# Kernel optimization log

Measured on AMD Instinct MI355X. Metric: run time of the kernel, lower is better.

Reference implementation:

```python
import jax, jax.numpy as jnp
import numpy as np

B, T = 2048, 512
H1, H2, H3 = 100, 60, 30


def _glorot(key, shape, fan):
    bound = 1.0 / np.sqrt(fan)
    return jax.random.uniform(key, shape, jnp.float32, -bound, bound)


def setup_inputs() -> dict:
    key = jax.random.key(0)
    ks = jax.random.split(key, 17)
    inp = {"x": jax.random.normal(ks[0], (B, T, 2), jnp.float32)}
    # layer 1: input 2 -> hidden 100
    inp["W_ih1"] = _glorot(ks[1], (H1, 2), H1)
    inp["W_hh1"] = _glorot(ks[2], (H1, H1), H1)
    inp["b_ih1"] = _glorot(ks[3], (H1,), H1)
    inp["b_hh1"] = _glorot(ks[4], (H1,), H1)
    # layer 2: 100 -> 60
    inp["W_ih2"] = _glorot(ks[5], (H2, H1), H2)
    inp["W_hh2"] = _glorot(ks[6], (H2, H2), H2)
    inp["b_ih2"] = _glorot(ks[7], (H2,), H2)
    inp["b_hh2"] = _glorot(ks[8], (H2,), H2)
    # layer 3: 60 -> 30
    inp["W_ih3"] = _glorot(ks[9], (H3, H2), H3)
    inp["W_hh3"] = _glorot(ks[10], (H3, H3), H3)
    inp["b_ih3"] = _glorot(ks[11], (H3,), H3)
    inp["b_hh3"] = _glorot(ks[12], (H3,), H3)
    # heads
    inp["W_o1"] = _glorot(ks[13], (10, H3), 10)
    inp["b_o1"] = _glorot(ks[14], (10,), 10)
    inp["W_o2"] = _glorot(ks[15], (2, 10), 2)
    inp["b_o2"] = _glorot(ks[16], (2,), 2)
    return inp


def rnn_layer(x, W_ih, W_hh, b_ih, b_hh):
    # x: [B, T, in]; precompute the time-parallel input projection once
    xp = jnp.einsum("bti,hi->bth", x, W_ih) + (b_ih + b_hh)  # [B, T, H]
    h0 = jnp.zeros((x.shape[0], W_hh.shape[0]), x.dtype)

    def step(h, xt):  # xt: [B, H]
        h = jnp.tanh(xt + h @ W_hh.T)
        return h, h

    _, ys = jax.lax.scan(step, h0, jnp.swapaxes(xp, 0, 1))  # [T, B, H]
    return jnp.swapaxes(ys, 0, 1)  # [B, T, H]


def reference(x, W_ih1, W_hh1, b_ih1, b_hh1, W_ih2, W_hh2, b_ih2, b_hh2,
              W_ih3, W_hh3, b_ih3, b_hh3, W_o1, b_o1, W_o2, b_o2):
    h = rnn_layer(x, W_ih1, W_hh1, b_ih1, b_hh1)
    h = rnn_layer(h, W_ih2, W_hh2, b_ih2, b_hh2)
    h = rnn_layer(h, W_ih3, W_hh3, b_ih3, b_hh3)
    o = jnp.einsum("bth,oh->bto", h, W_o1) + b_o1
    return jnp.einsum("bto,po->btp", o, W_o2) + b_o2  # [B, T, 2]
```

## Files before the change

### kernel.cpp

```cpp
#include <hip/hip_runtime.h>

typedef _Float16 v8hf __attribute__((ext_vector_type(8)));
typedef float    v4f  __attribute__((ext_vector_type(4)));

#define MFMA16(a, b, c) __builtin_amdgcn_mfma_f32_16x16x32_f16((a), (b), (c), 0, 0, 0)

#define TT 512
#define BT 16
#define NTH 1024
#define KS 2.8853900817779268f
#define CL 13.8498724f

#define H1R 0u
#define H2R 8192u
#define H3R 12288u
#define XST 14336u
#define ORG 47168u

__shared__ __align__(16) char SM[55360];

__device__ __forceinline__ v4f tanh4s(v4f z) {
    float z0 = __builtin_amdgcn_fmed3f(z[0], -CL, CL);
    float z1 = __builtin_amdgcn_fmed3f(z[1], -CL, CL);
    float z2 = __builtin_amdgcn_fmed3f(z[2], -CL, CL);
    float z3 = __builtin_amdgcn_fmed3f(z[3], -CL, CL);
    float a0 = __builtin_amdgcn_exp2f(z0) + 1.f;
    float a1 = __builtin_amdgcn_exp2f(z1) + 1.f;
    float a2 = __builtin_amdgcn_exp2f(z2) + 1.f;
    float a3 = __builtin_amdgcn_exp2f(z3) + 1.f;
    float P = a0 * a1, Q = a2 * a3;
    float R = __builtin_amdgcn_rcpf(P * Q);
    float iP = Q * R, iQ = P * R;
    v4f t;
    t[0] = 1.f - 2.f * (a1 * iP);
    t[1] = 1.f - 2.f * (a0 * iP);
    t[2] = 1.f - 2.f * (a3 * iQ);
    t[3] = 1.f - 2.f * (a2 * iQ);
    return t;
}

__device__ __forceinline__ unsigned pk2h(float a, float b) {
    union { _Float16 h[2]; unsigned u; } x;
    x.h[0] = (_Float16)a; x.h[1] = (_Float16)b;
    return x.u;
}

__global__ __launch_bounds__(NTH, 1)
void rnn3_nu(const float* __restrict__ xg,
             const float* __restrict__ Wih1, const float* __restrict__ Whh1,
             const float* __restrict__ bih1, const float* __restrict__ bhh1,
             const float* __restrict__ Wih2, const float* __restrict__ Whh2,
             const float* __restrict__ bih2, const float* __restrict__ bhh2,
             const float* __restrict__ Wih3, const float* __restrict__ Whh3,
             const float* __restrict__ bih3, const float* __restrict__ bhh3,
             const float* __restrict__ Wo1,  const float* __restrict__ bo1,
             const float* __restrict__ Wo2,  const float* __restrict__ bo2,
             float* __restrict__ outg)
{
    const int tid   = threadIdx.x;
    const int lane  = tid & 63;
    const int wid   = tid >> 6;
    const int col   = lane & 15;
    const int g     = lane >> 4;
    const int bbase = blockIdx.x * BT;
    const unsigned l16 = (unsigned)lane * 16u;

    {
        float4 z = {0.f, 0.f, 0.f, 0.f};
        for (int i = tid; i < 896; i += NTH) ((float4*)SM)[i] = z;
        for (int i = tid; i < BT * TT; i += NTH) {
            const int b = i >> 9, t = i & 511;
            float2 xv = *(const float2*)(xg + (size_t)(bbase + b) * (TT * 2) + 2 * t);
            *(unsigned*)(SM + XST + (unsigned)t * 64u + (unsigned)b * 4u) = pk2h(xv.x, xv.y);
        }
        if (tid < 16) *(unsigned*)(SM + XST + 512u * 64u + (unsigned)tid * 4u) = 0u;
    }

    v8hf WF[6];
    #pragma unroll
    for (int i = 0; i < 6; ++i) WF[i] = (v8hf)(_Float16)0.f;
    v4f BB0 = {0.f, 0.f, 0.f, 0.f}, BH = {0.f, 0.f, 0.f, 0.f};

    auto ldA = [&](const float* W, int rows, int cols, int jg, int kt) -> v8hf {
        v8hf r;
        #pragma unroll
        for (int e = 0; e < 8; ++e) {
            const int kl = 32 * kt + 16 * (e >> 2) + 4 * g + (e & 3);
            float v = (jg < rows && kl < cols) ? W[jg * cols + kl] * KS : 0.f;
            r[e] = (_Float16)v;
        }
        return r;
    };
    auto ldA1 = [&](int jg, int kt) -> v8hf {
        v8hf r;
        #pragma unroll
        for (int e = 0; e < 8; ++e) {
            const int kl = 32 * kt + 16 * (e >> 2) + 4 * g + (e & 3);
            float v = 0.f;
            if (jg < 100) {
                if (kl < 100)       v = Whh1[jg * 100 + kl];
                else if (kl == 112) v = Wih1[jg * 2];
                else if (kl == 113) v = Wih1[jg * 2 + 1];
            }
            r[e] = (_Float16)(v * KS);
        }
        return r;
    };
    auto mkbias = [&](const float* bi, const float* bh, int n, int t) -> v4f {
        v4f b;
        #pragma unroll
        for (int i = 0; i < 4; ++i) {
            const int j = 16 * t + 4 * g + i;
            b[i] = (j < n) ? KS * (bi[j] + bh[j]) : 0.f;
        }
        return b;
    };

    if (wid < 7) {
        #pragma unroll
        for (int kt = 0; kt < 4; ++kt) WF[kt] = ldA1(16 * wid + col, kt);
        BB0 = mkbias(bih1, bhh1, 100, wid);
    } else if (wid >= 8 && wid < 12) {
        const int j = 16 * (wid - 8) + col;
        #pragma unroll
        for (int kt = 0; kt < 4; ++kt) WF[kt] = ldA(Wih2, 60, 100, j, kt);
        WF[4] = ldA(Whh2, 60, 60, j, 0);
        WF[5] = ldA(Whh2, 60, 60, j, 1);
        BB0 = mkbias(bih2, bhh2, 60, wid - 8);
    } else if (wid == 12 || wid == 13) {
        const int j = 16 * (wid - 12) + col;
        WF[0] = ldA(Wih3, 30, 60, j, 0);
        WF[1] = ldA(Wih3, 30, 60, j, 1);
        WF[2] = ldA(Whh3, 30, 30, j, 0);
        BB0 = mkbias(bih3, bhh3, 30, wid - 12);
    } else if (wid == 14) {
        #pragma unroll
        for (int e = 0; e < 8; ++e) {
            const int kl = 16 * (e >> 2) + 4 * g + (e & 3);
            float v = 0.f;
            if (col < 2 && kl < 30) {
                #pragma unroll
                for (int u = 0; u < 10; ++u) v += Wo2[col * 10 + u] * Wo1[u * 30 + kl];
            }
            WF[0][e] = (_Float16)v;
        }
        #pragma unroll
        for (int i = 0; i < 4; ++i) {
            float bv = 0.f;
            if (g == 0 && i < 2) {
                bv = bo2[i];
                #pragma unroll
                for (int u = 0; u < 10; ++u) bv += Wo2[i * 10 + u] * bo1[u];
            }
            BH[i] = bv;
        }
    }

    __syncthreads();
    if (tid < 16)
        *(unsigned*)(SM + H1R + 4096u + 3072u + (unsigned)tid * 16u + 8u) =
            *(const unsigned*)(SM + XST + (unsigned)tid * 4u);
    __syncthreads();

    auto flushfn = [&](int tbase) {
        const unsigned rb = ORG + (((unsigned)tbase & 63u) >> 1) * 16u;
        #pragma unroll
        for (int jj = 0; jj < 4; ++jj) {
            const int f = lane + 64 * jj;
            const int b = f >> 4, k = f & 15;
            float4 v = *(const float4*)(SM + rb + (unsigned)b * 512u + (unsigned)k * 16u);
            *(float4*)(outg + ((size_t)(bbase + b) * TT + tbase) * 2 + 4 * k) = v;
        }
    };

    unsigned rO1 = H1R + 4096u, wO1 = H1R;
    unsigned rO2 = H2R + 2048u, wO2 = H2R;
    unsigned rO3 = H3R + 1024u, wO3 = H3R;
    const v4f z4 = {0.f, 0.f, 0.f, 0.f};

    for (int s = 0; s < TT + 3; ++s) {
        if (wid < 7) {
            if (s < TT) {
                v8hf S0 = *(const v8hf*)(SM + rO1 + l16);
                v8hf S1 = *(const v8hf*)(SM + rO1 + 1024u + l16);
                v8hf S2 = *(const v8hf*)(SM + rO1 + 2048u + l16);
                v8hf S3 = *(const v8hf*)(SM + rO1 + 3072u + l16);
                v4f p = BB0, q = z4;
                p = MFMA16(WF[0], S0, p); q = MFMA16(WF[1], S1, q);
                p = MFMA16(WF[2], S2, p); q = MFMA16(WF[3], S3, q);
                v4f r = tanh4s(p + q);
                uint2 wv; wv.x = pk2h(r[0], r[1]); wv.y = pk2h(r[2], r[3]);
                *(uint2*)(SM + wO1 + (unsigned)(wid >> 1) * 1024u + l16
                             + (unsigned)(wid & 1) * 8u) = wv;
            }
        } else if (wid == 7) {
            if (s < TT - 1) {
                unsigned xv = *(const unsigned*)(SM + XST + (unsigned)(s + 1) * 64u
                                                    + (unsigned)col * 4u);
                uint2 wv; wv.x = (g == 0) ? xv : 0u; wv.y = 0u;
                *(uint2*)(SM + wO1 + 3072u + l16 + 8u) = wv;
            }
        } else if (wid < 12) {
            if (s >= 1 && s <= TT) {
                v8hf G0 = *(const v8hf*)(SM + rO1 + l16);
                v8hf G1 = *(const v8hf*)(SM + rO1 + 1024u + l16);
                v8hf G2 = *(const v8hf*)(SM + rO1 + 2048u + l16);
                v8hf G3 = *(const v8hf*)(SM + rO1 + 3072u + l16);
                v8hf H0 = *(const v8hf*)(SM + rO2 + l16);
                v8hf H1 = *(const v8hf*)(SM + rO2 + 1024u + l16);
                v4f p = BB0, q = z4, r2 = z4;
                p  = MFMA16(WF[0], G0, p);
                q  = MFMA16(WF[1], G1, q);
                r2 = MFMA16(WF[4], H0, r2);
                p  = MFMA16(WF[2], G2, p);
                q  = MFMA16(WF[3], G3, q);
                r2 = MFMA16(WF[5], H1, r2);
                v4f r = tanh4s(p + q + r2);
                const int t2 = wid - 8;
                uint2 wv; wv.x = pk2h(r[0], r[1]); wv.y = pk2h(r[2], r[3]);
                *(uint2*)(SM + wO2 + (unsigned)(t2 >> 1) * 1024u + l16
                             + (unsigned)(t2 & 1) * 8u) = wv;
            }
        } else if (wid < 14) {
            if (s >= 2 && s <= TT + 1) {
                v8hf G0 = *(const v8hf*)(SM + rO2 + l16);
                v8hf G1 = *(const v8hf*)(SM + rO2 + 1024u + l16);
                v8hf C0 = *(const v8hf*)(SM + rO3 + l16);
                v4f p = BB0, q = z4, r2 = z4;
                p  = MFMA16(WF[0], G0, p);
                q  = MFMA16(WF[1], G1, q);
                r2 = MFMA16(WF[2], C0, r2);
                v4f r = tanh4s(p + q + r2);
                const int t3 = wid - 12;
                uint2 wv; wv.x = pk2h(r[0], r[1]); wv.y = pk2h(r[2], r[3]);
                *(uint2*)(SM + wO3 + l16 + (unsigned)(t3 & 1) * 8u) = wv;
            }
        } else if (wid == 14) {
            if (s >= 3 && s <= TT + 2) {
                v8hf C0 = *(const v8hf*)(SM + rO3 + l16);
                v4f o = BH;
                o = MFMA16(WF[0], C0, o);
                if (g == 0)
                    *(float2*)(SM + ORG + (unsigned)col * 512u
                                  + ((unsigned)(s - 3) & 63u) * 8u) =
                        make_float2(o[0], o[1]);
            }
        } else {
            if (s >= 35 && ((s - 35) & 31) == 0) flushfn(s - 35);
        }
        __syncthreads();
        rO1 ^= 4096u; wO1 ^= 4096u;
        rO2 ^= 2048u; wO2 ^= 2048u;
        rO3 ^= 1024u; wO3 ^= 1024u;
    }
    if (wid == 15) flushfn(480);
}

extern "C" void kernel_launch(void* const* d_in, const int* in_sizes, int n_in,
                              void* d_out, int out_size, void* d_ws, size_t ws_size,
                              hipStream_t stream) {
    (void)in_sizes; (void)n_in; (void)d_ws; (void)ws_size; (void)out_size;
    const float* x     = (const float*)d_in[0];
    const float* W_ih1 = (const float*)d_in[1];
    const float* W_hh1 = (const float*)d_in[2];
    const float* b_ih1 = (const float*)d_in[3];
    const float* b_hh1 = (const float*)d_in[4];
    const float* W_ih2 = (const float*)d_in[5];
    const float* W_hh2 = (const float*)d_in[6];
    const float* b_ih2 = (const float*)d_in[7];
    const float* b_hh2 = (const float*)d_in[8];
    const float* W_ih3 = (const float*)d_in[9];
    const float* W_hh3 = (const float*)d_in[10];
    const float* b_ih3 = (const float*)d_in[11];
    const float* b_hh3 = (const float*)d_in[12];
    const float* W_o1  = (const float*)d_in[13];
    const float* b_o1  = (const float*)d_in[14];
    const float* W_o2  = (const float*)d_in[15];
    const float* b_o2  = (const float*)d_in[16];
    float* out = (float*)d_out;

    rnn3_nu<<<2048 / BT, NTH, 0, stream>>>(
        x, W_ih1, W_hh1, b_ih1, b_hh1,
        W_ih2, W_hh2, b_ih2, b_hh2,
        W_ih3, W_hh3, b_ih3, b_hh3,
        W_o1, b_o1, W_o2, b_o2, out);
}
```

Baseline: 293.3 us.

## Replace lockstep block barriers with LDS flag-based producer/consumer pipeline across layers

Replaces the per-timestep __syncthreads lockstep schedule with per-role wave loops that coordinate through LDS atomic counters and 8-deep ring buffers for each layer's hidden state and the output staging area. Each layer's waves can run ahead of the downstream layers by up to several timesteps, which should hide the latency of waiting for the slowest role at every step. In exchange it adds spin-wait polling with s_sleep and atomic traffic on LDS, and it raises dynamic shared memory use to roughly 96 KB. The ordering relies on the correctness of the flag protocol.

```diff
diff --git a/kernel.cpp b/kernel.cpp
--- a/kernel.cpp
+++ b/kernel.cpp
@@ -12,12 +12,34 @@
 #define CL 13.8498724f
 
 #define H1R 0u
-#define H2R 8192u
-#define H3R 12288u
-#define XST 14336u
-#define ORG 47168u
-
-__shared__ __align__(16) char SM[55360];
+#define H2R 32768u
+#define H3R 49152u
+#define ORG 57344u
+#define XST 65536u
+#define FLG 98368u
+#define SMEMB 98432
+
+extern __shared__ __align__(16) char SMp[];
+
+#define F_C1 0
+#define F_R1 1
+#define F_C2 2
+#define F_R2 3
+#define F_C3 4
+#define F_R3 5
+#define F_CO 6
+#define F_FO 7
+
+__device__ __forceinline__ int* flagp(int i) { return (int*)(SMp + FLG) + i; }
+__device__ __forceinline__ void waitge(int i, int tgt) {
+    int* f = flagp(i);
+    while (__hip_atomic_load(f, __ATOMIC_ACQUIRE, __HIP_MEMORY_SCOPE_WORKGROUP) < tgt)
+        __builtin_amdgcn_s_sleep(1);
+}
+__device__ __forceinline__ void bump(int i, int v, int lane) {
+    if (lane == 0)
+        __hip_atomic_fetch_add(flagp(i), v, __ATOMIC_RELEASE, __HIP_MEMORY_SCOPE_WORKGROUP);
+}
 
 __device__ __forceinline__ v4f tanh4s(v4f z) {
     float z0 = __builtin_amdgcn_fmed3f(z[0], -CL, CL);
@@ -46,7 +68,7 @@
 }
 
 __global__ __launch_bounds__(NTH, 1)
-void rnn3_nu(const float* __restrict__ xg,
+void rnn3_pc(const float* __restrict__ xg,
              const float* __restrict__ Wih1, const float* __restrict__ Whh1,
              const float* __restrict__ bih1, const float* __restrict__ bhh1,
              const float* __restrict__ Wih2, const float* __restrict__ Whh2,
@@ -64,22 +86,23 @@
     const int g     = lane >> 4;
     const int bbase = blockIdx.x * BT;
     const unsigned l16 = (unsigned)lane * 16u;
-
-    {
-        float4 z = {0.f, 0.f, 0.f, 0.f};
-        for (int i = tid; i < 896; i += NTH) ((float4*)SM)[i] = z;
-        for (int i = tid; i < BT * TT; i += NTH) {
-            const int b = i >> 9, t = i & 511;
-            float2 xv = *(const float2*)(xg + (size_t)(bbase + b) * (TT * 2) + 2 * t);
-            *(unsigned*)(SM + XST + (unsigned)t * 64u + (unsigned)b * 4u) = pk2h(xv.x, xv.y);
-        }
-        if (tid < 16) *(unsigned*)(SM + XST + 512u * 64u + (unsigned)tid * 4u) = 0u;
+    const v4f z4 = {0.f, 0.f, 0.f, 0.f};
+
+    if (tid < 8) *flagp(tid) = 0;
+    for (int i = tid; i < 1024; i += NTH) ((float*)(SMp + H1R + 7u * 4096u))[i] = 0.f;
+    for (int i = tid; i < 512;  i += NTH) ((float*)(SMp + H2R + 7u * 2048u))[i] = 0.f;
+    for (int i = tid; i < 256;  i += NTH) ((float*)(SMp + H3R + 7u * 1024u))[i] = 0.f;
+    for (int i = tid; i < BT * TT; i += NTH) {
+        const int b = i >> 9, t = i & 511;
+        float2 xv = *(const float2*)(xg + (size_t)(bbase + b) * (TT * 2) + 2 * t);
+        *(unsigned*)(SMp + XST + (unsigned)t * 64u + (unsigned)b * 4u) = pk2h(xv.x, xv.y);
     }
-
-    v8hf WF[6];
-    #pragma unroll
-    for (int i = 0; i < 6; ++i) WF[i] = (v8hf)(_Float16)0.f;
-    v4f BB0 = {0.f, 0.f, 0.f, 0.f}, BH = {0.f, 0.f, 0.f, 0.f};
+    if (tid < 16) *(unsigned*)(SMp + XST + 512u * 64u + (unsigned)tid * 4u) = 0u;
+    __syncthreads();
+    if (tid < 16)
+        *(unsigned*)(SMp + H1R + 7u * 4096u + 3072u + (unsigned)tid * 16u + 8u) =
+            *(const unsigned*)(SMp + XST + (unsigned)tid * 4u);
+    __syncthreads();
 
     auto ldA = [&](const float* W, int rows, int cols, int jg, int kt) -> v8hf {
         v8hf r;
@@ -117,23 +140,101 @@
     };
 
     if (wid < 7) {
+        v8hf WF[4];
         #pragma unroll
         for (int kt = 0; kt < 4; ++kt) WF[kt] = ldA1(16 * wid + col, kt);
-        BB0 = mkbias(bih1, bhh1, 100, wid);
-    } else if (wid >= 8 && wid < 12) {
-        const int j = 16 * (wid - 8) + col;
+        v4f BB0 = mkbias(bih1, bhh1, 100, wid);
+        const unsigned woff = H1R + (unsigned)(wid >> 1) * 1024u + (unsigned)(wid & 1) * 8u + l16;
+        for (int t = 0; t < TT; ++t) {
+            if (t) waitge(F_C1, 8 * t);
+            const char* rb = SMp + H1R + (unsigned)((t + 7) & 7) * 4096u + l16;
+            v8hf S0 = *(const v8hf*)(rb);
+            v8hf S1 = *(const v8hf*)(rb + 1024);
+            v8hf S2 = *(const v8hf*)(rb + 2048);
+            v8hf S3 = *(const v8hf*)(rb + 3072);
+            v4f p = BB0, q = z4;
+            p = MFMA16(WF[0], S0, p); q = MFMA16(WF[1], S1, q);
+            p = MFMA16(WF[2], S2, p); q = MFMA16(WF[3], S3, q);
+            v4f r = tanh4s(p + q);
+            uint2 wv; wv.x = pk2h(r[0], r[1]); wv.y = pk2h(r[2], r[3]);
+            if (t >= 8) waitge(F_R1, 4 * (t - 7));
+            *(uint2*)(SMp + woff + (unsigned)(t & 7) * 4096u) = wv;
+            bump(F_C1, 1, lane);
+        }
+    } else if (wid == 7) {
+        for (int t = 0; t < TT; ++t) {
+            if (t) waitge(F_C1, 8 * t);
+            unsigned xv = *(const unsigned*)(SMp + XST + (unsigned)(t + 1) * 64u + (unsigned)col * 4u);
+            uint2 wv; wv.x = (g == 0) ? xv : 0u; wv.y = 0u;
+            if (t >= 8) waitge(F_R1, 4 * (t - 7));
+            *(uint2*)(SMp + H1R + (unsigned)(t & 7) * 4096u + 3072u + l16 + 8u) = wv;
+            bump(F_C1, 1, lane);
+        }
+    } else if (wid < 12) {
+        const int t2 = wid - 8;
+        const int j = 16 * t2 + col;
+        v8hf WF[6];
         #pragma unroll
         for (int kt = 0; kt < 4; ++kt) WF[kt] = ldA(Wih2, 60, 100, j, kt);
         WF[4] = ldA(Whh2, 60, 60, j, 0);
         WF[5] = ldA(Whh2, 60, 60, j, 1);
-        BB0 = mkbias(bih2, bhh2, 60, wid - 8);
-    } else if (wid == 12 || wid == 13) {
-        const int j = 16 * (wid - 12) + col;
+        v4f BB0 = mkbias(bih2, bhh2, 60, t2);
+        const unsigned woff = H2R + (unsigned)(t2 >> 1) * 1024u + (unsigned)(t2 & 1) * 8u + l16;
+        for (int t = 0; t < TT; ++t) {
+            waitge(F_C1, 8 * (t + 1));
+            if (t) waitge(F_C2, 4 * t);
+            const char* rb1 = SMp + H1R + (unsigned)(t & 7) * 4096u + l16;
+            const char* rb2 = SMp + H2R + (unsigned)((t + 7) & 7) * 2048u + l16;
+            v8hf G0 = *(const v8hf*)(rb1);
+            v8hf G1 = *(const v8hf*)(rb1 + 1024);
+            v8hf G2 = *(const v8hf*)(rb1 + 2048);
+            v8hf G3 = *(const v8hf*)(rb1 + 3072);
+            v8hf H0 = *(const v8hf*)(rb2);
+            v8hf H1 = *(const v8hf*)(rb2 + 1024);
+            bump(F_R1, 1, lane);
+            v4f p = BB0, q = z4, r2 = z4;
+            p  = MFMA16(WF[0], G0, p);
+            q  = MFMA16(WF[1], G1, q);
+            r2 = MFMA16(WF[4], H0, r2);
+            p  = MFMA16(WF[2], G2, p);
+            q  = MFMA16(WF[3], G3, q);
+            r2 = MFMA16(WF[5], H1, r2);
+            v4f r = tanh4s(p + q + r2);
+            uint2 wv; wv.x = pk2h(r[0], r[1]); wv.y = pk2h(r[2], r[3]);
+            if (t >= 8) waitge(F_R2, 2 * (t - 7));
+            *(uint2*)(SMp + woff + (unsigned)(t & 7) * 2048u) = wv;
+            bump(F_C2, 1, lane);
+        }
+    } else if (wid < 14) {
+        const int t3 = wid - 12;
+        const int j = 16 * t3 + col;
+        v8hf WF[3];
         WF[0] = ldA(Wih3, 30, 60, j, 0);
         WF[1] = ldA(Wih3, 30, 60, j, 1);
         WF[2] = ldA(Whh3, 30, 30, j, 0);
-        BB0 = mkbias(bih3, bhh3, 30, wid - 12);
+        v4f BB0 = mkbias(bih3, bhh3, 30, t3);
+        const unsigned woff = H3R + (unsigned)(t3 & 1) * 8u + l16;
+        for (int t = 0; t < TT; ++t) {
+            waitge(F_C2, 4 * (t + 1));
+            if (t) waitge(F_C3, 2 * t);
+            const char* rb2 = SMp + H2R + (unsigned)(t & 7) * 2048u + l16;
+            const char* rb3 = SMp + H3R + (unsigned)((t + 7) & 7) * 1024u + l16;
+            v8hf G0 = *(const v8hf*)(rb2);
+            v8hf G1 = *(const v8hf*)(rb2 + 1024);
+            v8hf C0 = *(const v8hf*)(rb3);
+            bump(F_R2, 1, lane);
+            v4f p = BB0, q = z4, r2 = z4;
+            p  = MFMA16(WF[0], G0, p);
+            q  = MFMA16(WF[1], G1, q);
+            r2 = MFMA16(WF[2], C0, r2);
+            v4f r = tanh4s(p + q + r2);
+            uint2 wv; wv.x = pk2h(r[0], r[1]); wv.y = pk2h(r[2], r[3]);
+            if (t >= 8) waitge(F_R3, t - 7);
+            *(uint2*)(SMp + woff + (unsigned)(t & 7) * 1024u) = wv;
+            bump(F_C3, 1, lane);
+        }
     } else if (wid == 14) {
+        v8hf We;
         #pragma unroll
         for (int e = 0; e < 8; ++e) {
             const int kl = 16 * (e >> 2) + 4 * g + (e & 3);
@@ -142,8 +243,9 @@
                 #pragma unroll
                 for (int u = 0; u < 10; ++u) v += Wo2[col * 10 + u] * Wo1[u * 30 + kl];
             }
-            WF[0][e] = (_Float16)v;
-        }
+            We[e] = (_Float16)v;
+        }
+        v4f BH;
         #pragma unroll
         for (int i = 0; i < 4; ++i) {
             float bv = 0.f;
@@ -154,106 +256,32 @@
             }
             BH[i] = bv;
         }
+        for (int t = 0; t < TT; ++t) {
+            waitge(F_C3, 2 * (t + 1));
+            v8hf C0 = *(const v8hf*)(SMp + H3R + (unsigned)(t & 7) * 1024u + l16);
+            bump(F_R3, 1, lane);
+            v4f o = BH;
+            o = MFMA16(We, C0, o);
+            if (t >= 64) waitge(F_FO, t - 63);
+            if (g == 0)
+                *(float2*)(SMp + ORG + (unsigned)col * 512u + ((unsigned)t & 63u) * 8u) =
+                    make_float2(o[0], o[1]);
+            bump(F_CO, 1, lane);
+        }
+    } else {
+        for (int tb = 0; tb <= 480; tb += 32) {
+            waitge(F_CO, tb + 32);
+            const unsigned rb = ORG + (((unsigned)tb & 63u) >> 1) * 16u;
+            #pragma unroll
+            for (int jj = 0; jj < 4; ++jj) {
+                const int f = lane + 64 * jj;
+                const int b = f >> 4, k = f & 15;
+                float4 v = *(const float4*)(SMp + rb + (unsigned)b * 512u + (unsigned)k * 16u);
+                *(float4*)(outg + ((size_t)(bbase + b) * TT + tb) * 2 + 4 * k) = v;
+            }
+            bump(F_FO, 32, lane);
+        }
     }
-
-    __syncthreads();
-    if (tid < 16)
-        *(unsigned*)(SM + H1R + 4096u + 3072u + (unsigned)tid * 16u + 8u) =
-            *(const unsigned*)(SM + XST + (unsigned)tid * 4u);
-    __syncthreads();
-
-    auto flushfn = [&](int tbase) {
-        const unsigned rb = ORG + (((unsigned)tbase & 63u) >> 1) * 16u;
-        #pragma unroll
-        for (int jj = 0; jj < 4; ++jj) {
-            const int f = lane + 64 * jj;
-            const int b = f >> 4, k = f & 15;
-            float4 v = *(const float4*)(SM + rb + (unsigned)b * 512u + (unsigned)k * 16u);
-            *(float4*)(outg + ((size_t)(bbase + b) * TT + tbase) * 2 + 4 * k) = v;
-        }
-    };
-
-    unsigned rO1 = H1R + 4096u, wO1 = H1R;
-    unsigned rO2 = H2R + 2048u, wO2 = H2R;
-    unsigned rO3 = H3R + 1024u, wO3 = H3R;
-    const v4f z4 = {0.f, 0.f, 0.f, 0.f};
-
-    for (int s = 0; s < TT + 3; ++s) {
-        if (wid < 7) {
-            if (s < TT) {
-                v8hf S0 = *(const v8hf*)(SM + rO1 + l16);
-                v8hf S1 = *(const v8hf*)(SM + rO1 + 1024u + l16);
-                v8hf S2 = *(const v8hf*)(SM + rO1 + 2048u + l16);
-                v8hf S3 = *(const v8hf*)(SM + rO1 + 3072u + l16);
-                v4f p = BB0, q = z4;
-                p = MFMA16(WF[0], S0, p); q = MFMA16(WF[1], S1, q);
-                p = MFMA16(WF[2], S2, p); q = MFMA16(WF[3], S3, q);
-                v4f r = tanh4s(p + q);
-                uint2 wv; wv.x = pk2h(r[0], r[1]); wv.y = pk2h(r[2], r[3]);
-                *(uint2*)(SM + wO1 + (unsigned)(wid >> 1) * 1024u + l16
-                             + (unsigned)(wid & 1) * 8u) = wv;
-            }
-        } else if (wid == 7) {
-            if (s < TT - 1) {
-                unsigned xv = *(const unsigned*)(SM + XST + (unsigned)(s + 1) * 64u
-                                                    + (unsigned)col * 4u);
-                uint2 wv; wv.x = (g == 0) ? xv : 0u; wv.y = 0u;
-                *(uint2*)(SM + wO1 + 3072u + l16 + 8u) = wv;
-            }
-        } else if (wid < 12) {
-            if (s >= 1 && s <= TT) {
-                v8hf G0 = *(const v8hf*)(SM + rO1 + l16);
-                v8hf G1 = *(const v8hf*)(SM + rO1 + 1024u + l16);
-                v8hf G2 = *(const v8hf*)(SM + rO1 + 2048u + l16);
-                v8hf G3 = *(const v8hf*)(SM + rO1 + 3072u + l16);
-                v8hf H0 = *(const v8hf*)(SM + rO2 + l16);
-                v8hf H1 = *(const v8hf*)(SM + rO2 + 1024u + l16);
-                v4f p = BB0, q = z4, r2 = z4;
-                p  = MFMA16(WF[0], G0, p);
-                q  = MFMA16(WF[1], G1, q);
-                r2 = MFMA16(WF[4], H0, r2);
-                p  = MFMA16(WF[2], G2, p);
-                q  = MFMA16(WF[3], G3, q);
-                r2 = MFMA16(WF[5], H1, r2);
-                v4f r = tanh4s(p + q + r2);
-                const int t2 = wid - 8;
-                uint2 wv; wv.x = pk2h(r[0], r[1]); wv.y = pk2h(r[2], r[3]);
-                *(uint2*)(SM + wO2 + (unsigned)(t2 >> 1) * 1024u + l16
-                             + (unsigned)(t2 & 1) * 8u) = wv;
-            }
-        } else if (wid < 14) {
-            if (s >= 2 && s <= TT + 1) {
-                v8hf G0 = *(const v8hf*)(SM + rO2 + l16);
-                v8hf G1 = *(const v8hf*)(SM + rO2 + 1024u + l16);
-                v8hf C0 = *(const v8hf*)(SM + rO3 + l16);
-                v4f p = BB0, q = z4, r2 = z4;
-                p  = MFMA16(WF[0], G0, p);
-                q  = MFMA16(WF[1], G1, q);
-                r2 = MFMA16(WF[2], C0, r2);
-                v4f r = tanh4s(p + q + r2);
-                const int t3 = wid - 12;
-                uint2 wv; wv.x = pk2h(r[0], r[1]); wv.y = pk2h(r[2], r[3]);
-                *(uint2*)(SM + wO3 + l16 + (unsigned)(t3 & 1) * 8u) = wv;
-            }
-        } else if (wid == 14) {
-            if (s >= 3 && s <= TT + 2) {
-                v8hf C0 = *(const v8hf*)(SM + rO3 + l16);
-                v4f o = BH;
-                o = MFMA16(WF[0], C0, o);
-                if (g == 0)
-                    *(float2*)(SM + ORG + (unsigned)col * 512u
-                                  + ((unsigned)(s - 3) & 63u) * 8u) =
-                        make_float2(o[0], o[1]);
-            }
-        } else {
-            if (s >= 35 && ((s - 35) & 31) == 0) flushfn(s - 35);
-        }
-        __syncthreads();
-        rO1 ^= 4096u; wO1 ^= 4096u;
-        rO2 ^= 2048u; wO2 ^= 2048u;
-        rO3 ^= 1024u; wO3 ^= 1024u;
-    }
-    if (wid == 15) flushfn(480);
 }
 
 extern "C" void kernel_launch(void* const* d_in, const int* in_sizes, int n_in,
@@ -279,7 +307,9 @@
     const float* b_o2  = (const float*)d_in[16];
     float* out = (float*)d_out;
 
-    rnn3_nu<<<2048 / BT, NTH, 0, stream>>>(
+    hipFuncSetAttribute((const void*)rnn3_pc,
+                        hipFuncAttributeMaxDynamicSharedMemorySize, SMEMB);
+    rnn3_pc<<<2048 / BT, NTH, SMEMB, stream>>>(
         x, W_ih1, W_hh1, b_ih1, b_hh1,
         W_ih2, W_hh2, b_ih2, b_hh2,
         W_ih3, W_hh3, b_ih3, b_hh3,
```

Result: slower. 331.2 us (+12.9%).
